# Performance work log

Measured on AMD Instinct MI355X. Metric: run time of the kernel, lower is better.

Reference implementation:

```python
import jax, jax.numpy as jnp
import numpy as np
import math

EPS = 1e-5

def _ln(x, w, b):
    m = jnp.mean(x, axis=-1, keepdims=True)
    v = jnp.mean((x - m) ** 2, axis=-1, keepdims=True)
    return (x - m) * jax.lax.rsqrt(v + EPS) * w + b

def setup_inputs() -> dict:
    key = jax.random.key(0)
    L, E, V, T, B = 8, 1024, 32000, 1024, 4
    ks = jax.random.split(key, 9)
    f = lambda k, s: jax.random.normal(k, s, dtype=jnp.float32) * 0.02
    return dict(
        idx=jax.random.randint(ks[0], (B, T), 0, V),
        wte=f(ks[1], (V, E)),
        wpe=f(ks[2], (T, E)),
        ln1_w=jnp.ones((L, E), jnp.float32), ln1_b=jnp.zeros((L, E), jnp.float32),
        attn_w=f(ks[3], (L, 3 * E, E)), attn_b=jnp.zeros((L, 3 * E), jnp.float32),
        proj_w=f(ks[4], (L, E, E)), proj_b=jnp.zeros((L, E), jnp.float32),
        ln2_w=jnp.ones((L, E), jnp.float32), ln2_b=jnp.zeros((L, E), jnp.float32),
        fc_w=f(ks[5], (L, 4 * E, E)), fc_b=jnp.zeros((L, 4 * E), jnp.float32),
        fc2_w=f(ks[6], (L, E, 4 * E)), fc2_b=jnp.zeros((L, E), jnp.float32),
        lnf_w=jnp.ones((E,), jnp.float32), lnf_b=jnp.zeros((E,), jnp.float32),
        lm_head_w=f(ks[7], (V, E)),
        n_head=16,
    )

def reference(idx, wte, wpe, ln1_w, ln1_b, attn_w, attn_b, proj_w, proj_b,
              ln2_w, ln2_b, fc_w, fc_b, fc2_w, fc2_b, lnf_w, lnf_b,
              lm_head_w, n_head):
    B, T = idx.shape
    E = wte.shape[1]
    H = int(n_head)
    hd = E // H
    scale = 1.0 / math.sqrt(hd)
    x = wte[idx] + wpe[:T]  # [B,T,E]
    causal = jnp.tril(jnp.ones((T, T), dtype=bool))
    neg_inf = jnp.float32(-jnp.inf)

    def body(x, p):
        l1w, l1b, Wa, ba, Wp, bp, l2w, l2b, Wf, bf, W2, b2 = p
        h = _ln(x, l1w, l1b)
        qkv = h @ Wa.T + ba  # [B,T,3E]
        q, k, v = jnp.split(qkv, 3, axis=-1)
        q = q.reshape(B, T, H, hd)
        k = k.reshape(B, T, H, hd)
        v = v.reshape(B, T, H, hd)
        att = jnp.einsum('bqhd,bkhd->bhqk', q, k) * scale
        att = jnp.where(causal, att, neg_inf)
        att = jax.nn.softmax(att, axis=-1)  # dropout is identity in eval
        y = jnp.einsum('bhqk,bkhd->bqhd', att, v).reshape(B, T, E)
        x = x + (y @ Wp.T + bp)
        h2 = _ln(x, l2w, l2b)
        mlp = jax.nn.gelu(h2 @ Wf.T + bf, approximate=False) @ W2.T + b2
        return x + mlp, None

    params = (ln1_w, ln1_b, attn_w, attn_b, proj_w, proj_b,
              ln2_w, ln2_b, fc_w, fc_b, fc2_w, fc2_b)
    x, _ = jax.lax.scan(body, x, params)
    x = _ln(x, lnf_w, lnf_b)
    logits = x @ lm_head_w.T  # [B,T,V]
    return logits
```

## Files before the change

kernel.cpp:

```cpp
#include <hip/hip_runtime.h>

typedef __bf16 bf16x8 __attribute__((ext_vector_type(8)));
typedef float  f32x4  __attribute__((ext_vector_type(4)));
typedef short  s16x8  __attribute__((ext_vector_type(8)));
typedef unsigned int u32;
#define AS1 __attribute__((address_space(1)))
#define AS3 __attribute__((address_space(3)))

#define E_ 1024
#define T_ 1024
#define B_ 4
#define L_ 8
#define V_ 32000
#define M_ (B_*T_)

static __device__ __forceinline__ ushort f2bf(float f) {
  return __builtin_bit_cast(ushort, (__bf16)f);
}
static __device__ __forceinline__ float bf2f(ushort u) {
  u32 t = (u32)u << 16;
  return __builtin_bit_cast(float, t);
}

static __device__ __forceinline__ bf16x8 dsr(const ushort* p) {
  u32 a = (u32)(size_t)(const AS3 ushort*)p;
  bf16x8 d;
  asm volatile("ds_read_b128 %0, %1" : "=v"(d) : "v"(a));
  return d;
}

__global__ __launch_bounds__(256) void castall_k(
    const float* __restrict__ a0, const float* __restrict__ a1,
    const float* __restrict__ a2, const float* __restrict__ a3,
    const float* __restrict__ a4,
    ushort* __restrict__ o0, ushort* __restrict__ o1, ushort* __restrict__ o2,
    ushort* __restrict__ o3, ushort* __restrict__ o4) {
  int bid = blockIdx.x;
  const float* in; ushort* out; int base;
  if (bid < 12288)      { in = a0; out = o0; base = bid; }
  else if (bid < 16384) { in = a1; out = o1; base = bid - 12288; }
  else if (bid < 32768) { in = a2; out = o2; base = bid - 16384; }
  else if (bid < 49152) { in = a3; out = o3; base = bid - 32768; }
  else                  { in = a4; out = o4; base = bid - 49152; }
  size_t i = ((size_t)base * 256 + threadIdx.x) * 8;
  float4 a = *(const float4*)(in + i);
  float4 b = *(const float4*)(in + i + 4);
  float v[8] = {a.x, a.y, a.z, a.w, b.x, b.y, b.z, b.w};
  union { s16x8 v; ushort u[8]; } pk;
  #pragma unroll
  for (int j = 0; j < 8; ++j) pk.u[j] = f2bf(v[j]);
  *(s16x8*)(out + i) = pk.v;
}

static __device__ __forceinline__ void ln_core(float4 v, int t,
    const float* __restrict__ w, const float* __restrict__ b,
    ushort* __restrict__ out, size_t row) {
  float s  = v.x + v.y + v.z + v.w;
  float s2 = v.x*v.x + v.y*v.y + v.z*v.z + v.w*v.w;
  #pragma unroll
  for (int o = 32; o > 0; o >>= 1) { s += __shfl_down(s, o); s2 += __shfl_down(s2, o); }
  __shared__ float sh[8];
  int wv = t >> 6;
  if ((t & 63) == 0) { sh[wv] = s; sh[4 + wv] = s2; }
  __syncthreads();
  s  = sh[0] + sh[1] + sh[2] + sh[3];
  s2 = sh[4] + sh[5] + sh[6] + sh[7];
  float mean = s * (1.f / E_);
  float var  = s2 * (1.f / E_) - mean * mean;
  float inv  = rsqrtf(var + 1e-5f);
  float4 wv4 = ((const float4*)w)[t];
  float4 bv4 = ((const float4*)b)[t];
  ushort* op = out + row * E_ + t * 4;
  op[0] = f2bf((v.x - mean) * inv * wv4.x + bv4.x);
  op[1] = f2bf((v.y - mean) * inv * wv4.y + bv4.y);
  op[2] = f2bf((v.z - mean) * inv * wv4.z + bv4.z);
  op[3] = f2bf((v.w - mean) * inv * wv4.w + bv4.w);
}

__global__ __launch_bounds__(256) void embedln_k(const int* __restrict__ idx,
    const float* __restrict__ wte, const float* __restrict__ wpe,
    const float* __restrict__ w, const float* __restrict__ b,
    float* __restrict__ x, ushort* __restrict__ out) {
  int row = blockIdx.x;
  int tok = idx[row];
  int t = row & (T_ - 1);
  int c = threadIdx.x;
  float4 a = ((const float4*)(wte + (size_t)tok * E_))[c];
  float4 p = ((const float4*)(wpe + (size_t)t * E_))[c];
  float4 v; v.x = a.x + p.x; v.y = a.y + p.y; v.z = a.z + p.z; v.w = a.w + p.w;
  ((float4*)(x + (size_t)row * E_))[c] = v;
  ln_core(v, c, w, b, out, (size_t)row);
}

__global__ __launch_bounds__(256) void ln_k(const float* __restrict__ x,
    const float* __restrict__ w, const float* __restrict__ b,
    ushort* __restrict__ out) {
  int row = blockIdx.x;
  int t = threadIdx.x;
  float4 v = ((const float4*)(x + (size_t)row * E_))[t];
  ln_core(v, t, w, b, out, (size_t)row);
}

__global__ __launch_bounds__(256) void redln_k(const ushort* __restrict__ p,
    const float* __restrict__ bias, float* __restrict__ x,
    const float* __restrict__ w, const float* __restrict__ b,
    ushort* __restrict__ out) {
  int row = blockIdx.x;
  int t = threadIdx.x;
  float4 v = ((const float4*)(x + (size_t)row * E_))[t];
  float4 bb = ((const float4*)bias)[t];
  v.x += bb.x; v.y += bb.y; v.z += bb.z; v.w += bb.w;
  #pragma unroll
  for (int sk = 0; sk < 4; ++sk) {
    const ushort* q = p + ((size_t)sk * M_ + row) * E_ + t * 4;
    v.x += bf2f(q[0]); v.y += bf2f(q[1]); v.z += bf2f(q[2]); v.w += bf2f(q[3]);
  }
  ((float4*)(x + (size_t)row * E_))[t] = v;
  ln_core(v, t, w, b, out, (size_t)row);
}

template<int BUF, int MH, int NH, int RA, int RB, int VM, typename F>
static __device__ __forceinline__ void ph8(
    const ushort* AL, const ushort* BL,
    bf16x8 (&av)[2][4][2], bf16x8 (&bv)[2][2][2],
    int arow, int brow, int ca0, int ca1, f32x4 (&acc)[8][4], F&& stage) {
  if (RA) {
    #pragma unroll
    for (int mfi = 0; mfi < 4; ++mfi) {
      av[MH][mfi][0] = dsr(&AL[(BUF*2+MH)*8192 + arow + mfi*1024 + ca0]);
      av[MH][mfi][1] = dsr(&AL[(BUF*2+MH)*8192 + arow + mfi*1024 + ca1]);
    }
  }
  if (RB) {
    #pragma unroll
    for (int nfi = 0; nfi < 2; ++nfi) {
      bv[NH][nfi][0] = dsr(&BL[(BUF*2+NH)*8192 + brow + nfi*1024 + ca0]);
      bv[NH][nfi][1] = dsr(&BL[(BUF*2+NH)*8192 + brow + nfi*1024 + ca1]);
    }
  }
  stage();
  __builtin_amdgcn_s_barrier();
  asm volatile("s_waitcnt lgkmcnt(0)");
  __builtin_amdgcn_sched_barrier(0);
  __builtin_amdgcn_s_setprio(1);
  #pragma unroll
  for (int ks = 0; ks < 2; ++ks)
    #pragma unroll
    for (int mfi = 0; mfi < 4; ++mfi)
      #pragma unroll
      for (int nfi = 0; nfi < 2; ++nfi)
        acc[MH*4+mfi][NH*2+nfi] = __builtin_amdgcn_mfma_f32_16x16x32_bf16(
            av[MH][mfi][ks], bv[NH][nfi][ks], acc[MH*4+mfi][NH*2+nfi], 0, 0, 0);
  __builtin_amdgcn_s_setprio(0);
  if (VM) asm volatile("s_waitcnt vmcnt(4)");
  __builtin_amdgcn_s_barrier();
  __builtin_amdgcn_sched_barrier(0);
}

#define GLDS(src, dst) __builtin_amdgcn_global_load_lds((const AS1 u32*)(src), (AS3 u32*)(dst), 16, 0, 0)
#define STAGE_A(b, s, t) do { \
  GLDS(ap##s##_0 + (size_t)(t)*64, &AL[((b)*2+(s))*8192 + w*512]); \
  GLDS(ap##s##_1 + (size_t)(t)*64, &AL[((b)*2+(s))*8192 + 4096 + w*512]); } while(0)
#define STAGE_B(b, s, t) do { \
  GLDS(bp##s##_0 + (size_t)(t)*64, &BL[((b)*2+(s))*8192 + w*512]); \
  GLDS(bp##s##_1 + (size_t)(t)*64, &BL[((b)*2+(s))*8192 + 4096 + w*512]); } while(0)

__global__ __launch_bounds__(512, 2)
void gemm8_lm(const ushort* __restrict__ A, const ushort* __restrict__ W,
              float* __restrict__ outf) {
  const int N = V_, K = E_, Kst = E_;
  __shared__ __align__(16) ushort AL[32768];
  __shared__ __align__(16) ushort BL[32768];
  int id  = blockIdx.x;
  int nwg = gridDim.x;
  int swz = (id & 7) * (nwg >> 3) + (id >> 3);
  int bx = swz >> 4, by = swz & 15;
  int bm = by * 256, bn = bx * 256;
  int tid = threadIdx.x;
  int w = tid >> 6, lane = tid & 63;
  int wm = w >> 2, wn = w & 3;
  int g = lane >> 4, lr = lane & 15;
  int sl8 = lane >> 3, sc = lane & 7;
  int cg8 = (sc ^ sl8) * 8;

  int r0 = w * 8 + sl8;
  const ushort* ap0_0 = A + (size_t)(bm +       0 + r0) * Kst + cg8;
  const ushort* ap0_1 = A + (size_t)(bm + 128 + 0 + r0) * Kst + cg8;
  const ushort* ap1_0 = A + (size_t)(bm +      64 + r0) * Kst + cg8;
  const ushort* ap1_1 = A + (size_t)(bm + 128 + 64 + r0) * Kst + cg8;
  int sr0 = r0, sr1 = 64 + r0;
  const ushort* bp0_0 = W + (size_t)(bn + (sr0 >> 5) * 64 +  0 + (sr0 & 31)) * Kst + cg8;
  const ushort* bp0_1 = W + (size_t)(bn + (sr1 >> 5) * 64 +  0 + (sr1 & 31)) * Kst + cg8;
  const ushort* bp1_0 = W + (size_t)(bn + (sr0 >> 5) * 64 + 32 + (sr0 & 31)) * Kst + cg8;
  const ushort* bp1_1 = W + (size_t)(bn + (sr1 >> 5) * 64 + 32 + (sr1 & 31)) * Kst + cg8;

  int NT = K >> 6;
  int NITER = NT >> 1;
  int arow = (wm * 64 + lr) * 64;
  int brow = (wn * 32 + lr) * 64;
  int ca0 = ((0 + g) ^ (lr & 7)) * 8;
  int ca1 = ((4 + g) ^ (lr & 7)) * 8;
  f32x4 acc[8][4] = {};
  bf16x8 av[2][4][2], bv[2][2][2];

  STAGE_A(0, 0, 0); STAGE_A(0, 1, 0); STAGE_B(0, 0, 0); STAGE_B(0, 1, 0);
  STAGE_A(1, 0, 1); STAGE_B(1, 0, 1);
  asm volatile("s_waitcnt vmcnt(0)" ::: "memory");
  __builtin_amdgcn_s_barrier();
  __builtin_amdgcn_sched_barrier(0);

  for (int i = 0; i < NITER; ++i) {
    int t1 = 2 * i + 1;
    int t2 = 2 * i + 2; if (t2 > NT - 1) t2 = NT - 1;
    int t3 = 2 * i + 3; if (t3 > NT - 1) t3 = NT - 1;
    ph8<0,0,0,1,1,0>(AL, BL, av, bv, arow, brow, ca0, ca1, acc, [&]{ STAGE_A(1, 1, t1); });
    ph8<0,0,1,0,1,0>(AL, BL, av, bv, arow, brow, ca0, ca1, acc, [&]{ STAGE_B(1, 1, t1); });
    ph8<0,1,1,1,0,0>(AL, BL, av, bv, arow, brow, ca0, ca1, acc, [&]{ STAGE_A(0, 0, t2); });
    ph8<0,1,0,0,0,1>(AL, BL, av, bv, arow, brow, ca0, ca1, acc, [&]{ STAGE_B(0, 0, t2); });
    ph8<1,0,0,1,1,0>(AL, BL, av, bv, arow, brow, ca0, ca1, acc, [&]{ STAGE_A(0, 1, t2); });
    ph8<1,0,1,0,1,0>(AL, BL, av, bv, arow, brow, ca0, ca1, acc, [&]{ STAGE_B(0, 1, t2); });
    ph8<1,1,1,1,0,0>(AL, BL, av, bv, arow, brow, ca0, ca1, acc, [&]{ STAGE_A(1, 0, t3); });
    ph8<1,1,0,0,0,1>(AL, BL, av, bv, arow, brow, ca0, ca1, acc, [&]{ STAGE_B(1, 0, t3); });
  }

  #pragma unroll
  for (int mf = 0; mf < 8; ++mf)
    #pragma unroll
    for (int reg = 0; reg < 4; ++reg) {
      int row = bm + wm * 128 + mf * 16 + g * 4 + reg;
      #pragma unroll
      for (int nf = 0; nf < 4; ++nf) {
        int col = bn + wn * 64 + nf * 16 + lr;
        outf[(size_t)row * N + col] = acc[mf][nf][reg];
      }
    }
}

template<int EPI>
static __device__ __forceinline__
void gbt2_body(const ushort* __restrict__ A, const ushort* __restrict__ W,
               const float* __restrict__ bias, const float* __restrict__ res,
               float* __restrict__ outf, ushort* __restrict__ outh,
               ushort* __restrict__ qb, ushort* __restrict__ kb, ushort* __restrict__ vb,
               int N, int K, int Kst, int gx) {
  __shared__ __align__(16) ushort As[128 * 64];
  __shared__ __align__(16) ushort Ws[128 * 64];
  int id  = blockIdx.x;
  int nwg = gridDim.x;
  int swz = (id & 7) * (nwg >> 3) + (id >> 3);
  int sk = 0;
  if (EPI == 4) { sk = swz >> 8; swz &= 255; }
  int bx = swz / 32, by = swz & 31;
  int bm = by * 128, bn = bx * 128;
  int tid  = threadIdx.x;
  int wave = tid >> 6, lane = tid & 63;
  int wr = wave >> 1, wc = wave & 1;
  int g  = lane >> 4, lr = lane & 15;
  int sl8 = lane >> 3, sc = lane & 7;
  int cg8 = (sc ^ sl8) * 8;
  int r0 = wave * 8 + sl8;

  const ushort* ap = A + (size_t)sk * 1024 + (size_t)(bm + r0) * Kst + cg8;
  const ushort* wp = W + (size_t)sk * 1024 + (size_t)(bn + r0) * Kst + cg8;
  f32x4 acc[4][4] = {};

  for (int k0 = 0; k0 < K; k0 += 64) {
    #pragma unroll
    for (int j = 0; j < 4; ++j) {
      GLDS(ap + (size_t)(j * 32) * Kst + k0, &As[(wave * 8 + j * 32) * 64]);
      GLDS(wp + (size_t)(j * 32) * Kst + k0, &Ws[(wave * 8 + j * 32) * 64]);
    }
    __syncthreads();
    #pragma unroll
    for (int ks = 0; ks < 2; ++ks) {
      int ca = ((ks * 4 + g) ^ (lr & 7)) * 8;
      bf16x8 af[4], bfr[4];
      #pragma unroll
      for (int f = 0; f < 4; ++f) {
        af[f]  = __builtin_bit_cast(bf16x8, *(const s16x8*)&As[(wr * 64 + f * 16 + lr) * 64 + ca]);
        bfr[f] = __builtin_bit_cast(bf16x8, *(const s16x8*)&Ws[(wc * 64 + f * 16 + lr) * 64 + ca]);
      }
      #pragma unroll
      for (int mf = 0; mf < 4; ++mf)
        #pragma unroll
        for (int nf = 0; nf < 4; ++nf)
          acc[mf][nf] = __builtin_amdgcn_mfma_f32_16x16x32_bf16(af[mf], bfr[nf], acc[mf][nf], 0, 0, 0);
    }
    __syncthreads();
  }

  if (EPI == 3 && (bn >> 10) == 2) {
    #pragma unroll
    for (int mf = 0; mf < 4; ++mf) {
      int row = bm + wr * 64 + mf * 16 + g * 4;
      int b = row >> 10, t = row & 1023;
      #pragma unroll
      for (int nf = 0; nf < 4; ++nf) {
        int col = bn + wc * 64 + nf * 16 + lr;
        int cc = col & 1023;
        int h = cc >> 6, d = cc & 63;
        float bs = bias[col];
        union { ushort u[4]; uint2 v; } pk4;
        #pragma unroll
        for (int reg = 0; reg < 4; ++reg) pk4.u[reg] = f2bf(acc[mf][nf][reg] + bs);
        *(uint2*)&vb[((size_t)(b * 16 + h) * 64 + d) * T_ + t] = pk4.v;
      }
    }
    return;
  }

  ushort* dst = nullptr; float scl = 1.f;
  if (EPI == 3) {
    int sec = bn >> 10;
    dst = (sec == 0) ? qb : kb;
    scl = (sec == 0) ? 0.125f : 1.f;
  }
  #pragma unroll
  for (int mf = 0; mf < 4; ++mf)
    #pragma unroll
    for (int reg = 0; reg < 4; ++reg) {
      int row = bm + wr * 64 + mf * 16 + g * 4 + reg;
      #pragma unroll
      for (int nf = 0; nf < 4; ++nf) {
        int col = bn + wc * 64 + nf * 16 + lr;
        float v = acc[mf][nf][reg];
        if (EPI != 4) v += bias[col];
        if (EPI == 1) {
          outf[(size_t)row * N + col] = v + res[(size_t)row * N + col];
        } else if (EPI == 2) {
          float gl = 0.5f * v * (1.f + erff(v * 0.70710678118654752f));
          outh[(size_t)row * N + col] = f2bf(gl);
        } else if (EPI == 4) {
          outh[((size_t)sk * M_ + row) * N + col] = f2bf(v);
        } else {
          int b = row >> 10, t = row & 1023;
          int cc = col & 1023;
          int h = cc >> 6, d = cc & 63;
          dst[((size_t)(b * 16 + h) * T_ + t) * 64 + d] = f2bf(v * scl);
        }
      }
    }
}

__global__ __launch_bounds__(256, 4)
void gbt2_qkv(const ushort* A, const ushort* W, const float* bias,
              ushort* qb, ushort* kb, ushort* vtb) {
  gbt2_body<3>(A, W, bias, nullptr, nullptr, nullptr, qb, kb, vtb, 3 * E_, E_, E_, 24);
}
__global__ __launch_bounds__(256, 4)
void gbt2_fc(const ushort* A, const ushort* W, const float* bias, ushort* outh) {
  gbt2_body<2>(A, W, bias, nullptr, nullptr, outh, nullptr, nullptr, nullptr, 4 * E_, E_, E_, 32);
}
__global__ __launch_bounds__(256, 4)
void gbt2_sk(const ushort* A, const ushort* W, ushort* pbh) {
  gbt2_body<4>(A, W, nullptr, nullptr, nullptr, pbh, nullptr, nullptr, nullptr, E_, E_, 4 * E_, 8);
}
__global__ __launch_bounds__(256, 4)
void gbt2_proj(const ushort* A, const ushort* W, const float* bias,
               const float* res, float* outf) {
  gbt2_body<1>(A, W, bias, res, outf, nullptr, nullptr, nullptr, nullptr, E_, E_, E_, 8);
}

static __device__ __forceinline__ void sm_step(
    f32x4 (&s)[4], float& m, float& l, f32x4 (&acc)[4], bf16x8 (&ap)[2],
    int qrow, int kbase0, bool diag, int g) {
  if (diag) {
    #pragma unroll
    for (int nf = 0; nf < 4; ++nf)
      #pragma unroll
      for (int reg = 0; reg < 4; ++reg)
        if (kbase0 + nf * 16 + g * 4 + reg > qrow) s[nf][reg] = -INFINITY;
  }
  float pmax = s[0][0];
  #pragma unroll
  for (int nf = 0; nf < 4; ++nf)
    #pragma unroll
    for (int reg = 0; reg < 4; ++reg) pmax = fmaxf(pmax, s[nf][reg]);
  pmax = fmaxf(pmax, __shfl_xor(pmax, 16));
  pmax = fmaxf(pmax, __shfl_xor(pmax, 32));
  if (__any(pmax > m + 8.f)) {
    float mn = fmaxf(m, pmax);
    float corr = __expf(m - mn);
    m = mn; l *= corr;
    #pragma unroll
    for (int reg = 0; reg < 4; ++reg) {
      float cc = __shfl(corr, g * 4 + reg);
      #pragma unroll
      for (int nfd = 0; nfd < 4; ++nfd) acc[nfd][reg] *= cc;
    }
  }
  float ps = 0.f;
  union { bf16x8 v[2]; ushort u[16]; } pk;
  #pragma unroll
  for (int nf = 0; nf < 4; ++nf)
    #pragma unroll
    for (int reg = 0; reg < 4; ++reg) {
      float pv = __expf(s[nf][reg] - m);
      ps += pv;
      pk.u[nf * 4 + reg] = f2bf(pv);
    }
  ps += __shfl_xor(ps, 16);
  ps += __shfl_xor(ps, 32);
  l += ps;
  ap[0] = pk.v[0];
  ap[1] = pk.v[1];
}

__global__ __launch_bounds__(256) void attn4_k(const ushort* __restrict__ Qg,
    const ushort* __restrict__ Kg, const ushort* __restrict__ Vg,
    ushort* __restrict__ y) {
  __shared__ __align__(16) ushort KL[2][4096];
  __shared__ __align__(16) ushort VL[2][4096];
  int bh = blockIdx.x;
  int qt = blockIdx.y;
  int tid = threadIdx.x, w = tid >> 6, lane = tid & 63;
  int g = lane >> 4, lr = lane & 15;
  int sl8 = lane >> 3, sc = lane & 7;
  int cg8 = (sc ^ sl8) * 8;
  int qbase = qt * 128 + w * 32;

  const ushort* kbase = Kg + (size_t)bh * T_ * 64;
  const ushort* vbase = Vg + (size_t)bh * 64 * T_;

  bf16x8 aq[2][2];
  #pragma unroll
  for (int st = 0; st < 2; ++st) {
    const ushort* qp = Qg + ((size_t)bh * T_ + qbase + st * 16 + lr) * 64;
    aq[st][0] = __builtin_bit_cast(bf16x8, *(const s16x8*)(qp + g * 8));
    aq[st][1] = __builtin_bit_cast(bf16x8, *(const s16x8*)(qp + 32 + g * 8));
  }

  f32x4 accO[2][4] = {};
  float m0 = -INFINITY, m1 = -INFINITY, l0 = 0.f, l1 = 0.f;

  int nkt_blk = 2 * qt + 2;
  int nw = ((qbase + 31) >> 6) + 1;
  int r8 = w * 8 + sl8;

  #define STG_KV(buf, kt) do { \
    _Pragma("unroll") \
    for (int j_ = 0; j_ < 2; ++j_) { \
      GLDS(kbase + (size_t)((kt) * 64 + j_ * 32 + r8) * 64 + cg8, &KL[buf][(j_ * 32 + w * 8) * 64]); \
      GLDS(vbase + (size_t)(j_ * 32 + r8) * T_ + (kt) * 64 + cg8, &VL[buf][(j_ * 32 + w * 8) * 64]); \
    } \
  } while (0)

  STG_KV(0, 0);
  __syncthreads();

  for (int kt = 0; kt < nkt_blk; ++kt) {
    int cbuf = kt & 1;
    if (kt + 1 < nkt_blk) STG_KV(cbuf ^ 1, kt + 1);

    if (kt < nw) {
      bool diag = (kt == nw - 1);
      f32x4 s0[4] = {}, s1[4] = {};
      #pragma unroll
      for (int ks = 0; ks < 2; ++ks)
        #pragma unroll
        for (int nf = 0; nf < 4; ++nf) {
          int row = nf * 16 + lr;
          bf16x8 ak = __builtin_bit_cast(bf16x8,
              *(const s16x8*)&KL[cbuf][row * 64 + (((ks * 4 + g) ^ (lr & 7)) * 8)]);
          s0[nf] = __builtin_amdgcn_mfma_f32_16x16x32_bf16(ak, aq[0][ks], s0[nf], 0, 0, 0);
          s1[nf] = __builtin_amdgcn_mfma_f32_16x16x32_bf16(ak, aq[1][ks], s1[nf], 0, 0, 0);
        }

      bf16x8 ap0[2], ap1[2];
      sm_step(s0, m0, l0, accO[0], ap0, qbase + 0 * 16 + lr, kt * 64, diag, g);
      sm_step(s1, m1, l1, accO[1], ap1, qbase + 1 * 16 + lr, kt * 64, diag, g);

      #pragma unroll
      for (int ks = 0; ks < 2; ++ks)
        #pragma unroll
        for (int nfd = 0; nfd < 4; ++nfd) {
          int row = nfd * 16 + lr;
          int c1 = ks * 4 + (g >> 1), sub = (g & 1) * 4;
          uint2 lo = *(const uint2*)&VL[cbuf][row * 64 + ((c1 ^ (lr & 7)) * 8 + sub)];
          uint2 hi = *(const uint2*)&VL[cbuf][row * 64 + (((c1 + 2) ^ (lr & 7)) * 8 + sub)];
          union { uint4 u; bf16x8 v; } bb;
          bb.u = make_uint4(lo.x, lo.y, hi.x, hi.y);
          accO[0][nfd] = __builtin_amdgcn_mfma_f32_16x16x32_bf16(ap0[ks], bb.v, accO[0][nfd], 0, 0, 0);
          accO[1][nfd] = __builtin_amdgcn_mfma_f32_16x16x32_bf16(ap1[ks], bb.v, accO[1][nfd], 0, 0, 0);
        }
    }
    __syncthreads();
  }

  int b = bh >> 4, h = bh & 15;
  float li0 = 1.f / l0, li1 = 1.f / l1;
  #pragma unroll
  for (int st = 0; st < 2; ++st) {
    float lsrc = (st == 0) ? li0 : li1;
    #pragma unroll
    for (int reg = 0; reg < 4; ++reg) {
      float inv = __shfl(lsrc, g * 4 + reg);
      size_t row = (size_t)b * T_ + qbase + st * 16 + g * 4 + reg;
      #pragma unroll
      for (int nfd = 0; nfd < 4; ++nfd)
        y[row * E_ + h * 64 + nfd * 16 + lr] = f2bf(accO[st][nfd][reg] * inv);
    }
  }
  #undef STG_KV
}

extern "C" void kernel_launch(void* const* d_in, const int* in_sizes, int n_in,
                              void* d_out, int out_size, void* d_ws, size_t ws_size,
                              hipStream_t stream) {
  const int*   idx   = (const int*)  d_in[0];
  const float* wte   = (const float*)d_in[1];
  const float* wpe   = (const float*)d_in[2];
  const float* ln1w  = (const float*)d_in[3];
  const float* ln1b  = (const float*)d_in[4];
  const float* attnw = (const float*)d_in[5];
  const float* attnb = (const float*)d_in[6];
  const float* projw = (const float*)d_in[7];
  const float* projb = (const float*)d_in[8];
  const float* ln2w  = (const float*)d_in[9];
  const float* ln2b  = (const float*)d_in[10];
  const float* fcw   = (const float*)d_in[11];
  const float* fcb   = (const float*)d_in[12];
  const float* fc2w  = (const float*)d_in[13];
  const float* fc2b  = (const float*)d_in[14];
  const float* lnfw  = (const float*)d_in[15];
  const float* lnfb  = (const float*)d_in[16];
  const float* lmw   = (const float*)d_in[17];
  float* out = (float*)d_out;

  char* p = (char*)d_ws;
  auto take = [&](size_t bytes) { char* r = p; p += (bytes + 255) & ~(size_t)255; return r; };
  ushort* wb_attn = (ushort*)take((size_t)L_ * 3 * E_ * E_ * 2);
  ushort* wb_proj = (ushort*)take((size_t)L_ * E_ * E_ * 2);
  ushort* wb_fc   = (ushort*)take((size_t)L_ * 4 * E_ * E_ * 2);
  ushort* wb_fc2  = (ushort*)take((size_t)L_ * E_ * 4 * E_ * 2);
  ushort* wb_lm   = (ushort*)take((size_t)V_ * E_ * 2);
  float*  x       = (float*) take((size_t)M_ * E_ * 4);
  ushort* hbuf    = (ushort*)take((size_t)M_ * E_ * 2);
  ushort* qb      = (ushort*)take((size_t)B_ * 16 * T_ * 64 * 2);
  ushort* kbuf    = (ushort*)take((size_t)B_ * 16 * T_ * 64 * 2);
  ushort* vtb     = (ushort*)take((size_t)B_ * 16 * T_ * 64 * 2);
  ushort* ybuf    = (ushort*)take((size_t)M_ * E_ * 2);
  ushort* mlp     = (ushort*)take((size_t)M_ * 4 * E_ * 2);
  ushort* pbh     = (ushort*)take((size_t)4 * M_ * E_ * 2);

  castall_k<<<65152, 256, 0, stream>>>(attnw, projw, fcw, fc2w, lmw,
                                       wb_attn, wb_proj, wb_fc, wb_fc2, wb_lm);
  embedln_k<<<M_, 256, 0, stream>>>(idx, wte, wpe, ln1w, ln1b, x, hbuf);

  for (int l = 0; l < L_; ++l) {
    gbt2_qkv<<<24 * 32, 256, 0, stream>>>(
        hbuf, wb_attn + (size_t)l * 3 * E_ * E_, attnb + l * 3 * E_, qb, kbuf, vtb);
    attn4_k<<<dim3(B_ * 16, T_ / 128), 256, 0, stream>>>(qb, kbuf, vtb, ybuf);
    gbt2_proj<<<8 * 32, 256, 0, stream>>>(
        ybuf, wb_proj + (size_t)l * E_ * E_, projb + l * E_, x, x);
    ln_k<<<M_, 256, 0, stream>>>(x, ln2w + l * E_, ln2b + l * E_, hbuf);
    gbt2_fc<<<32 * 32, 256, 0, stream>>>(
        hbuf, wb_fc + (size_t)l * 4 * E_ * E_, fcb + l * 4 * E_, mlp);
    gbt2_sk<<<4 * 8 * 32, 256, 0, stream>>>(mlp, wb_fc2 + (size_t)l * E_ * 4 * E_, pbh);
    if (l < L_ - 1)
      redln_k<<<M_, 256, 0, stream>>>(pbh, fc2b + l * E_, x,
                                      ln1w + (l + 1) * E_, ln1b + (l + 1) * E_, hbuf);
    else
      redln_k<<<M_, 256, 0, stream>>>(pbh, fc2b + l * E_, x, lnfw, lnfb, hbuf);
  }
  gemm8_lm<<<(V_ / 256) * (M_ / 256), 512, 0, stream>>>(hbuf, wb_lm, out);
}
```

Measured before the change: 2.190 ms.

## Simplify LM-head GEMM to single-buffer loop and widen attention blocks to 512 threads

The LM-head GEMM drops its 8-phase double-buffered pipeline with hand-scheduled ds_reads and priority hints. In its place is a simple single-buffer K loop: stage a 256x64 tile, read fragments, run the MFMAs, then sync. LDS use is halved and launch bounds now allow 4 blocks per CU, so occupancy replaces explicit overlap as the way to hide latency. The attention kernel moves to 512 threads covering 256 query rows per block, which halves the grid and lets each K/V tile stage serve more warps. The main risks are losing load/compute overlap in the GEMM and a longer causal tail imbalance in attention.

```diff
diff --git a/kernel.cpp b/kernel.cpp
--- a/kernel.cpp
+++ b/kernel.cpp
@@ -20,13 +20,6 @@
 static __device__ __forceinline__ float bf2f(ushort u) {
   u32 t = (u32)u << 16;
   return __builtin_bit_cast(float, t);
-}
-
-static __device__ __forceinline__ bf16x8 dsr(const ushort* p) {
-  u32 a = (u32)(size_t)(const AS3 ushort*)p;
-  bf16x8 d;
-  asm volatile("ds_read_b128 %0, %1" : "=v"(d) : "v"(a));
-  return d;
 }
 
 __global__ __launch_bounds__(256) void castall_k(
@@ -119,58 +112,14 @@
   ln_core(v, t, w, b, out, (size_t)row);
 }
 
-template<int BUF, int MH, int NH, int RA, int RB, int VM, typename F>
-static __device__ __forceinline__ void ph8(
-    const ushort* AL, const ushort* BL,
-    bf16x8 (&av)[2][4][2], bf16x8 (&bv)[2][2][2],
-    int arow, int brow, int ca0, int ca1, f32x4 (&acc)[8][4], F&& stage) {
-  if (RA) {
-    #pragma unroll
-    for (int mfi = 0; mfi < 4; ++mfi) {
-      av[MH][mfi][0] = dsr(&AL[(BUF*2+MH)*8192 + arow + mfi*1024 + ca0]);
-      av[MH][mfi][1] = dsr(&AL[(BUF*2+MH)*8192 + arow + mfi*1024 + ca1]);
-    }
-  }
-  if (RB) {
-    #pragma unroll
-    for (int nfi = 0; nfi < 2; ++nfi) {
-      bv[NH][nfi][0] = dsr(&BL[(BUF*2+NH)*8192 + brow + nfi*1024 + ca0]);
-      bv[NH][nfi][1] = dsr(&BL[(BUF*2+NH)*8192 + brow + nfi*1024 + ca1]);
-    }
-  }
-  stage();
-  __builtin_amdgcn_s_barrier();
-  asm volatile("s_waitcnt lgkmcnt(0)");
-  __builtin_amdgcn_sched_barrier(0);
-  __builtin_amdgcn_s_setprio(1);
-  #pragma unroll
-  for (int ks = 0; ks < 2; ++ks)
-    #pragma unroll
-    for (int mfi = 0; mfi < 4; ++mfi)
-      #pragma unroll
-      for (int nfi = 0; nfi < 2; ++nfi)
-        acc[MH*4+mfi][NH*2+nfi] = __builtin_amdgcn_mfma_f32_16x16x32_bf16(
-            av[MH][mfi][ks], bv[NH][nfi][ks], acc[MH*4+mfi][NH*2+nfi], 0, 0, 0);
-  __builtin_amdgcn_s_setprio(0);
-  if (VM) asm volatile("s_waitcnt vmcnt(4)");
-  __builtin_amdgcn_s_barrier();
-  __builtin_amdgcn_sched_barrier(0);
-}
-
 #define GLDS(src, dst) __builtin_amdgcn_global_load_lds((const AS1 u32*)(src), (AS3 u32*)(dst), 16, 0, 0)
-#define STAGE_A(b, s, t) do { \
-  GLDS(ap##s##_0 + (size_t)(t)*64, &AL[((b)*2+(s))*8192 + w*512]); \
-  GLDS(ap##s##_1 + (size_t)(t)*64, &AL[((b)*2+(s))*8192 + 4096 + w*512]); } while(0)
-#define STAGE_B(b, s, t) do { \
-  GLDS(bp##s##_0 + (size_t)(t)*64, &BL[((b)*2+(s))*8192 + w*512]); \
-  GLDS(bp##s##_1 + (size_t)(t)*64, &BL[((b)*2+(s))*8192 + 4096 + w*512]); } while(0)
-
-__global__ __launch_bounds__(512, 2)
-void gemm8_lm(const ushort* __restrict__ A, const ushort* __restrict__ W,
+
+__global__ __launch_bounds__(512, 4)
+void gemm9_lm(const ushort* __restrict__ A, const ushort* __restrict__ W,
               float* __restrict__ outf) {
-  const int N = V_, K = E_, Kst = E_;
-  __shared__ __align__(16) ushort AL[32768];
-  __shared__ __align__(16) ushort BL[32768];
+  const int N = V_, K = E_;
+  __shared__ __align__(16) ushort AL[16384];
+  __shared__ __align__(16) ushort BL[16384];
   int id  = blockIdx.x;
   int nwg = gridDim.x;
   int swz = (id & 7) * (nwg >> 3) + (id >> 3);
@@ -180,48 +129,52 @@
   int w = tid >> 6, lane = tid & 63;
   int wm = w >> 2, wn = w & 3;
   int g = lane >> 4, lr = lane & 15;
-  int sl8 = lane >> 3, sc = lane & 7;
-  int cg8 = (sc ^ sl8) * 8;
-
-  int r0 = w * 8 + sl8;
-  const ushort* ap0_0 = A + (size_t)(bm +       0 + r0) * Kst + cg8;
-  const ushort* ap0_1 = A + (size_t)(bm + 128 + 0 + r0) * Kst + cg8;
-  const ushort* ap1_0 = A + (size_t)(bm +      64 + r0) * Kst + cg8;
-  const ushort* ap1_1 = A + (size_t)(bm + 128 + 64 + r0) * Kst + cg8;
-  int sr0 = r0, sr1 = 64 + r0;
-  const ushort* bp0_0 = W + (size_t)(bn + (sr0 >> 5) * 64 +  0 + (sr0 & 31)) * Kst + cg8;
-  const ushort* bp0_1 = W + (size_t)(bn + (sr1 >> 5) * 64 +  0 + (sr1 & 31)) * Kst + cg8;
-  const ushort* bp1_0 = W + (size_t)(bn + (sr0 >> 5) * 64 + 32 + (sr0 & 31)) * Kst + cg8;
-  const ushort* bp1_1 = W + (size_t)(bn + (sr1 >> 5) * 64 + 32 + (sr1 & 31)) * Kst + cg8;
-
-  int NT = K >> 6;
-  int NITER = NT >> 1;
-  int arow = (wm * 64 + lr) * 64;
-  int brow = (wn * 32 + lr) * 64;
-  int ca0 = ((0 + g) ^ (lr & 7)) * 8;
-  int ca1 = ((4 + g) ^ (lr & 7)) * 8;
+  int rr = tid >> 3;
+  int sc = tid & 7;
+  int cg8 = (sc ^ (rr & 7)) * 8;
+  int wl8 = (w * 8) * 64;
+
+  const ushort* ap = A + (size_t)(bm + rr) * K + cg8;
+  const ushort* wp = W + (size_t)(bn + rr) * K + cg8;
   f32x4 acc[8][4] = {};
-  bf16x8 av[2][4][2], bv[2][2][2];
-
-  STAGE_A(0, 0, 0); STAGE_A(0, 1, 0); STAGE_B(0, 0, 0); STAGE_B(0, 1, 0);
-  STAGE_A(1, 0, 1); STAGE_B(1, 0, 1);
-  asm volatile("s_waitcnt vmcnt(0)" ::: "memory");
-  __builtin_amdgcn_s_barrier();
-  __builtin_amdgcn_sched_barrier(0);
-
-  for (int i = 0; i < NITER; ++i) {
-    int t1 = 2 * i + 1;
-    int t2 = 2 * i + 2; if (t2 > NT - 1) t2 = NT - 1;
-    int t3 = 2 * i + 3; if (t3 > NT - 1) t3 = NT - 1;
-    ph8<0,0,0,1,1,0>(AL, BL, av, bv, arow, brow, ca0, ca1, acc, [&]{ STAGE_A(1, 1, t1); });
-    ph8<0,0,1,0,1,0>(AL, BL, av, bv, arow, brow, ca0, ca1, acc, [&]{ STAGE_B(1, 1, t1); });
-    ph8<0,1,1,1,0,0>(AL, BL, av, bv, arow, brow, ca0, ca1, acc, [&]{ STAGE_A(0, 0, t2); });
-    ph8<0,1,0,0,0,1>(AL, BL, av, bv, arow, brow, ca0, ca1, acc, [&]{ STAGE_B(0, 0, t2); });
-    ph8<1,0,0,1,1,0>(AL, BL, av, bv, arow, brow, ca0, ca1, acc, [&]{ STAGE_A(0, 1, t2); });
-    ph8<1,0,1,0,1,0>(AL, BL, av, bv, arow, brow, ca0, ca1, acc, [&]{ STAGE_B(0, 1, t2); });
-    ph8<1,1,1,1,0,0>(AL, BL, av, bv, arow, brow, ca0, ca1, acc, [&]{ STAGE_A(1, 0, t3); });
-    ph8<1,1,0,0,0,1>(AL, BL, av, bv, arow, brow, ca0, ca1, acc, [&]{ STAGE_B(1, 0, t3); });
-  }
+
+  #define STG9(k0) do { \
+    _Pragma("unroll") \
+    for (int j_ = 0; j_ < 4; ++j_) { \
+      GLDS(ap + (size_t)(j_ * 64) * K + (k0), &AL[j_ * 4096 + wl8]); \
+      GLDS(wp + (size_t)(j_ * 64) * K + (k0), &BL[j_ * 4096 + wl8]); \
+    } \
+  } while (0)
+
+  STG9(0);
+  __syncthreads();
+  for (int k0 = 0; k0 < K; k0 += 64) {
+    bf16x8 av[8][2], bv[4][2];
+    #pragma unroll
+    for (int ks = 0; ks < 2; ++ks) {
+      int ca = ((ks * 4 + g) ^ (lr & 7)) * 8;
+      #pragma unroll
+      for (int mf = 0; mf < 8; ++mf)
+        av[mf][ks] = __builtin_bit_cast(bf16x8,
+            *(const s16x8*)&AL[(wm * 128 + mf * 16 + lr) * 64 + ca]);
+      #pragma unroll
+      for (int nf = 0; nf < 4; ++nf)
+        bv[nf][ks] = __builtin_bit_cast(bf16x8,
+            *(const s16x8*)&BL[(wn * 64 + nf * 16 + lr) * 64 + ca]);
+    }
+    #pragma unroll
+    for (int ks = 0; ks < 2; ++ks)
+      #pragma unroll
+      for (int mf = 0; mf < 8; ++mf)
+        #pragma unroll
+        for (int nf = 0; nf < 4; ++nf)
+          acc[mf][nf] = __builtin_amdgcn_mfma_f32_16x16x32_bf16(
+              av[mf][ks], bv[nf][ks], acc[mf][nf], 0, 0, 0);
+    __syncthreads();
+    if (k0 + 64 < K) STG9(k0 + 64);
+    __syncthreads();
+  }
+  #undef STG9
 
   #pragma unroll
   for (int mf = 0; mf < 8; ++mf)
@@ -406,7 +359,7 @@
   ap[1] = pk.v[1];
 }
 
-__global__ __launch_bounds__(256) void attn4_k(const ushort* __restrict__ Qg,
+__global__ __launch_bounds__(512) void attn8_k(const ushort* __restrict__ Qg,
     const ushort* __restrict__ Kg, const ushort* __restrict__ Vg,
     ushort* __restrict__ y) {
   __shared__ __align__(16) ushort KL[2][4096];
@@ -415,9 +368,11 @@
   int qt = blockIdx.y;
   int tid = threadIdx.x, w = tid >> 6, lane = tid & 63;
   int g = lane >> 4, lr = lane & 15;
-  int sl8 = lane >> 3, sc = lane & 7;
-  int cg8 = (sc ^ sl8) * 8;
-  int qbase = qt * 128 + w * 32;
+  int rr = tid >> 3;
+  int sc = tid & 7;
+  int cg8 = (sc ^ (rr & 7)) * 8;
+  int wl8 = (w * 8) * 64;
+  int qbase = qt * 256 + w * 32;
 
   const ushort* kbase = Kg + (size_t)bh * T_ * 64;
   const ushort* vbase = Vg + (size_t)bh * 64 * T_;
@@ -433,16 +388,12 @@
   f32x4 accO[2][4] = {};
   float m0 = -INFINITY, m1 = -INFINITY, l0 = 0.f, l1 = 0.f;
 
-  int nkt_blk = 2 * qt + 2;
+  int nkt_blk = 4 * qt + 4;
   int nw = ((qbase + 31) >> 6) + 1;
-  int r8 = w * 8 + sl8;
 
   #define STG_KV(buf, kt) do { \
-    _Pragma("unroll") \
-    for (int j_ = 0; j_ < 2; ++j_) { \
-      GLDS(kbase + (size_t)((kt) * 64 + j_ * 32 + r8) * 64 + cg8, &KL[buf][(j_ * 32 + w * 8) * 64]); \
-      GLDS(vbase + (size_t)(j_ * 32 + r8) * T_ + (kt) * 64 + cg8, &VL[buf][(j_ * 32 + w * 8) * 64]); \
-    } \
+    GLDS(kbase + (size_t)((kt) * 64 + rr) * 64 + cg8, &KL[buf][wl8]); \
+    GLDS(vbase + (size_t)rr * T_ + (kt) * 64 + cg8, &VL[buf][wl8]); \
   } while (0)
 
   STG_KV(0, 0);
@@ -550,7 +501,7 @@
   for (int l = 0; l < L_; ++l) {
     gbt2_qkv<<<24 * 32, 256, 0, stream>>>(
         hbuf, wb_attn + (size_t)l * 3 * E_ * E_, attnb + l * 3 * E_, qb, kbuf, vtb);
-    attn4_k<<<dim3(B_ * 16, T_ / 128), 256, 0, stream>>>(qb, kbuf, vtb, ybuf);
+    attn8_k<<<dim3(B_ * 16, T_ / 256), 512, 0, stream>>>(qb, kbuf, vtb, ybuf);
     gbt2_proj<<<8 * 32, 256, 0, stream>>>(
         ybuf, wb_proj + (size_t)l * E_ * E_, projb + l * E_, x, x);
     ln_k<<<M_, 256, 0, stream>>>(x, ln2w + l * E_, ln2b + l * E_, hbuf);
@@ -563,5 +514,5 @@
     else
       redln_k<<<M_, 256, 0, stream>>>(pbh, fc2b + l * E_, x, lnfw, lnfb, hbuf);
   }
-  gemm8_lm<<<(V_ / 256) * (M_ / 256), 512, 0, stream>>>(hbuf, wb_lm, out);
-}
+  gemm9_lm<<<(V_ / 256) * (M_ / 256), 512, 0, stream>>>(hbuf, wb_lm, out);
+}
```

Result: slower. 3.530 ms (+61.2%).
